# Kernel optimization log

Measured on AMD Instinct MI355X. Metric: run time of the kernel, lower is better.

The kernel has to match this reference:

```python
import jax, jax.numpy as jnp
import numpy as np

TEMPERATURE = 8.0  # sqrt(d_head=64), from init_kwargs
NEG_INF = -1e9


def setup_inputs() -> dict:
    key = jax.random.key(0)
    k1, k2, k3, k4 = jax.random.split(key, 4)
    B, H, N, D = 2, 16, 2048, 64
    q = jax.random.normal(k1, (B, H, N, D), dtype=jnp.float32)
    k = jax.random.normal(k2, (B, H, N, D), dtype=jnp.float32)
    v = jax.random.normal(k3, (B, H, N, D), dtype=jnp.float32)
    mask = jax.random.randint(k4, (B, 1, N), 0, 2, dtype=jnp.int32)
    return {"q": q, "k": k, "v": v, "mask": mask}


def reference(q, k, v, mask):
    # scores: [B,H,N,N]
    attn = jnp.einsum("bhqd,bhkd->bhqk", q / TEMPERATURE, k)
    # symmetric padding mask: masked if row OR col token is masked
    m = mask.astype(attn.dtype)            # [B,1,N]
    row = m[:, :, :, None]                 # [B,1,N,1]
    col = m[:, :, None, :]                 # [B,1,1,N]
    sym = 1.0 - (1.0 - row) * (1.0 - col)  # [B,1,N,N], broadcasts over H
    attn = jnp.where(sym == 1.0, NEG_INF, attn)
    attn = jax.nn.softmax(attn, axis=-1)
    output = jnp.einsum("bhqk,bhkd->bhqd", attn, v)
    return output, attn
```

## Files before the change

kernel.cpp:

```cpp
#include <hip/hip_runtime.h>

typedef _Float16 half8 __attribute__((ext_vector_type(8)));
typedef _Float16 half4v __attribute__((ext_vector_type(4)));
typedef float f32x4 __attribute__((ext_vector_type(4)));

__global__ __launch_bounds__(256, 2)
void attn_fused(const float* __restrict__ qg_, const float* __restrict__ kg_,
                const float* __restrict__ vg_, const int* __restrict__ mg_,
                float* __restrict__ outg_, float* __restrict__ attng_)
{
    constexpr int N = 2048, D = 64, TM = 128, BK = 128, NCH = 16;
    constexpr int QS = 72, KS = 72, VTS = 136, PS = 72;
    constexpr float INVN = 1.0f / 2048.0f;

    __shared__ _Float16 Qs[TM * QS];
    __shared__ _Float16 Ksh[BK * KS];
    __shared__ _Float16 Vts[D * VTS];
    __shared__ _Float16 Ps[TM * PS];
    __shared__ unsigned char cm[N];

    const int tid  = threadIdx.x;
    const int wid  = tid >> 6;
    const int lane = tid & 63;
    const int quad = lane >> 4;
    const int l15  = lane & 15;

    const int bh = blockIdx.x & 31;
    const int qt = blockIdx.x >> 5;
    const int b  = bh >> 4;

    const float* qg = qg_ + ((size_t)bh * N + qt * TM) * D;
    const float* kg = kg_ + (size_t)bh * N * D;
    const float* vg = vg_ + (size_t)bh * N * D;
    const int*   mg = mg_ + (size_t)b * N;
    float* attng = attng_ + ((size_t)bh * N + (size_t)qt * TM) * N;
    float* outg  = outg_  + ((size_t)bh * N + qt * TM) * D;

#pragma unroll
    for (int i = 0; i < 8; ++i) {
        int f = tid + 256 * i;
        int row = f >> 4, d = (f & 15) * 4;
        float4 x = *reinterpret_cast<const float4*>(qg + (size_t)row * D + d);
        half4v hv;
        hv[0] = (_Float16)(x.x * 0.125f);
        hv[1] = (_Float16)(x.y * 0.125f);
        hv[2] = (_Float16)(x.z * 0.125f);
        hv[3] = (_Float16)(x.w * 0.125f);
        *reinterpret_cast<half4v*>(&Qs[row * QS + d]) = hv;
        cm[f] = (unsigned char)(mg[f] ? 0 : 1);
    }

    float rowm[2][4];
#pragma unroll
    for (int mb = 0; mb < 2; ++mb)
#pragma unroll
        for (int r = 0; r < 4; ++r) {
            int row = qt * TM + wid * 32 + mb * 16 + quad * 4 + r;
            rowm[mb][r] = (float)mg[row];
        }

    __syncthreads();

    half8 qf[2][2];
#pragma unroll
    for (int mb = 0; mb < 2; ++mb)
#pragma unroll
        for (int ks = 0; ks < 2; ++ks)
            qf[mb][ks] = *reinterpret_cast<half8*>(
                &Qs[(wid * 32 + mb * 16 + l15) * QS + ks * 32 + quad * 8]);

    float lsum[2][4] = {{0,0,0,0},{0,0,0,0}};

    for (int kc = 0; kc < NCH; ++kc) {
        __syncthreads();
#pragma unroll
        for (int i = 0; i < 8; ++i) {
            int f = tid + 256 * i;
            int row = f >> 4, d = (f & 15) * 4;
            float4 x = *reinterpret_cast<const float4*>(kg + (size_t)(kc * BK + row) * D + d);
            half4v hv;
            hv[0] = (_Float16)x.x; hv[1] = (_Float16)x.y;
            hv[2] = (_Float16)x.z; hv[3] = (_Float16)x.w;
            *reinterpret_cast<half4v*>(&Ksh[row * KS + d]) = hv;
        }
        __syncthreads();

#pragma unroll
        for (int mb = 0; mb < 2; ++mb) {
#pragma unroll
            for (int nb = 0; nb < 8; ++nb) {
                f32x4 acc = {0.f, 0.f, 0.f, 0.f};
#pragma unroll
                for (int ks = 0; ks < 2; ++ks) {
                    half8 bf = *reinterpret_cast<half8*>(
                        &Ksh[(nb * 16 + l15) * KS + ks * 32 + quad * 8]);
                    acc = __builtin_amdgcn_mfma_f32_16x16x32_f16(qf[mb][ks], bf, acc, 0, 0, 0);
                }
                float cmf = (float)cm[kc * BK + nb * 16 + l15];
#pragma unroll
                for (int r = 0; r < 4; ++r)
                    lsum[mb][r] += cmf * __expf(acc[r]);
            }
        }
    }

#pragma unroll
    for (int mb = 0; mb < 2; ++mb)
#pragma unroll
        for (int r = 0; r < 4; ++r) {
            float s = lsum[mb][r];
            s += __shfl_xor(s, 1, 64);
            s += __shfl_xor(s, 2, 64);
            s += __shfl_xor(s, 4, 64);
            s += __shfl_xor(s, 8, 64);
            lsum[mb][r] = s;
        }

    float rscale[2][4], radd[2][4];
#pragma unroll
    for (int mb = 0; mb < 2; ++mb)
#pragma unroll
        for (int r = 0; r < 4; ++r) {
            bool uni = (rowm[mb][r] != 0.0f) || !(lsum[mb][r] > 0.0f);
            rscale[mb][r] = uni ? 0.0f : 1.0f / lsum[mb][r];
            radd[mb][r]   = uni ? INVN : 0.0f;
        }

    f32x4 Oacc[2][4];
#pragma unroll
    for (int mb = 0; mb < 2; ++mb)
#pragma unroll
        for (int nd = 0; nd < 4; ++nd)
            Oacc[mb][nd] = (f32x4){0.f, 0.f, 0.f, 0.f};

    for (int kc = 0; kc < NCH; ++kc) {
        __syncthreads();
#pragma unroll
        for (int i = 0; i < 8; ++i) {
            int f = tid + 256 * i;
            int row = f >> 4, d = (f & 15) * 4;
            float4 x = *reinterpret_cast<const float4*>(kg + (size_t)(kc * BK + row) * D + d);
            half4v hv;
            hv[0] = (_Float16)x.x; hv[1] = (_Float16)x.y;
            hv[2] = (_Float16)x.z; hv[3] = (_Float16)x.w;
            *reinterpret_cast<half4v*>(&Ksh[row * KS + d]) = hv;
        }
#pragma unroll
        for (int rr = 0; rr < 4; ++rr) {
            int key0 = rr * 32 + wid * 8;
            half8 hh;
#pragma unroll
            for (int j = 0; j < 8; ++j)
                hh[j] = (_Float16)vg[(size_t)(kc * BK + key0 + j) * D + lane];
            *reinterpret_cast<half8*>(&Vts[lane * VTS + key0]) = hh;
        }
        __syncthreads();

        f32x4 S[2][8];
#pragma unroll
        for (int mb = 0; mb < 2; ++mb)
#pragma unroll
            for (int nb = 0; nb < 8; ++nb) {
                f32x4 acc = {0.f, 0.f, 0.f, 0.f};
#pragma unroll
                for (int ks = 0; ks < 2; ++ks) {
                    half8 bf = *reinterpret_cast<half8*>(
                        &Ksh[(nb * 16 + l15) * KS + ks * 32 + quad * 8]);
                    acc = __builtin_amdgcn_mfma_f32_16x16x32_f16(qf[mb][ks], bf, acc, 0, 0, 0);
                }
                S[mb][nb] = acc;
            }

#pragma unroll
        for (int h = 0; h < 2; ++h) {
#pragma unroll
            for (int nb2 = 0; nb2 < 4; ++nb2) {
                int nb = h * 4 + nb2;
                int col = kc * BK + nb * 16 + l15;
                float cmf = (float)cm[col];
#pragma unroll
                for (int mb = 0; mb < 2; ++mb) {
#pragma unroll
                    for (int r = 0; r < 4; ++r) {
                        float p = cmf * __expf(S[mb][nb][r]) * rscale[mb][r] + radd[mb][r];
                        attng[(size_t)(wid * 32 + mb * 16 + quad * 4 + r) * N + col] = p;
                        Ps[(wid * 32 + mb * 16 + quad * 4 + r) * PS + nb2 * 16 + l15] = (_Float16)p;
                    }
                }
            }
            asm volatile("s_waitcnt lgkmcnt(0)" ::: "memory");
#pragma unroll
            for (int ks = 0; ks < 2; ++ks) {
                half8 af[2];
#pragma unroll
                for (int mb = 0; mb < 2; ++mb)
                    af[mb] = *reinterpret_cast<half8*>(
                        &Ps[(wid * 32 + mb * 16 + l15) * PS + ks * 32 + quad * 8]);
#pragma unroll
                for (int nd = 0; nd < 4; ++nd) {
                    half8 bf = *reinterpret_cast<half8*>(
                        &Vts[(nd * 16 + l15) * VTS + h * 64 + ks * 32 + quad * 8]);
#pragma unroll
                    for (int mb = 0; mb < 2; ++mb)
                        Oacc[mb][nd] = __builtin_amdgcn_mfma_f32_16x16x32_f16(af[mb], bf, Oacc[mb][nd], 0, 0, 0);
                }
            }
        }
    }

#pragma unroll
    for (int mb = 0; mb < 2; ++mb)
#pragma unroll
        for (int nd = 0; nd < 4; ++nd)
#pragma unroll
            for (int r = 0; r < 4; ++r)
                outg[(size_t)(wid * 32 + mb * 16 + quad * 4 + r) * D + nd * 16 + l15] =
                    Oacc[mb][nd][r];
}

extern "C" void kernel_launch(void* const* d_in, const int* in_sizes, int n_in,
                              void* d_out, int out_size, void* d_ws, size_t ws_size,
                              hipStream_t stream) {
    const float* q   = (const float*)d_in[0];
    const float* k   = (const float*)d_in[1];
    const float* v   = (const float*)d_in[2];
    const int*   msk = (const int*)d_in[3];
    float* out  = (float*)d_out;
    float* attn = out + (size_t)2 * 16 * 2048 * 64;
    dim3 grid(512), block(256);
    hipLaunchKernelGGL(attn_fused, grid, block, 0, stream, q, k, v, msk, out, attn);
}
```

Baseline: 671.6 us.

## Vectorize attention-matrix stores via LDS restaging and use exp2 with folded log2e

Attention probabilities are now written to global memory as 16-byte nontemporal vector stores, read back from the fp16 P tile in shared memory, instead of scalar strided stores straight from MFMA registers. The log2(e) factor is folded into the Q scale so the exponentials use the hardware exp2 instruction. The output stores also become nontemporal. The stored attention values are now rounded through fp16, which loses precision in the returned attn matrix and could fail a tight tolerance.

```diff
diff --git a/kernel.cpp b/kernel.cpp
--- a/kernel.cpp
+++ b/kernel.cpp
@@ -3,6 +3,12 @@
 typedef _Float16 half8 __attribute__((ext_vector_type(8)));
 typedef _Float16 half4v __attribute__((ext_vector_type(4)));
 typedef float f32x4 __attribute__((ext_vector_type(4)));
+
+#if __has_builtin(__builtin_amdgcn_exp2f)
+#define EXP2F(x) __builtin_amdgcn_exp2f(x)
+#else
+#define EXP2F(x) exp2f(x)
+#endif
 
 __global__ __launch_bounds__(256, 2)
 void attn_fused(const float* __restrict__ qg_, const float* __restrict__ kg_,
@@ -12,6 +18,7 @@
     constexpr int N = 2048, D = 64, TM = 128, BK = 128, NCH = 16;
     constexpr int QS = 72, KS = 72, VTS = 136, PS = 72;
     constexpr float INVN = 1.0f / 2048.0f;
+    constexpr float QSCALE = 1.44269504088896340736f * 0.125f;
 
     __shared__ _Float16 Qs[TM * QS];
     __shared__ _Float16 Ksh[BK * KS];
@@ -42,10 +49,10 @@
         int row = f >> 4, d = (f & 15) * 4;
         float4 x = *reinterpret_cast<const float4*>(qg + (size_t)row * D + d);
         half4v hv;
-        hv[0] = (_Float16)(x.x * 0.125f);
-        hv[1] = (_Float16)(x.y * 0.125f);
-        hv[2] = (_Float16)(x.z * 0.125f);
-        hv[3] = (_Float16)(x.w * 0.125f);
+        hv[0] = (_Float16)(x.x * QSCALE);
+        hv[1] = (_Float16)(x.y * QSCALE);
+        hv[2] = (_Float16)(x.z * QSCALE);
+        hv[3] = (_Float16)(x.w * QSCALE);
         *reinterpret_cast<half4v*>(&Qs[row * QS + d]) = hv;
         cm[f] = (unsigned char)(mg[f] ? 0 : 1);
     }
@@ -99,7 +106,7 @@
                 float cmf = (float)cm[kc * BK + nb * 16 + l15];
 #pragma unroll
                 for (int r = 0; r < 4; ++r)
-                    lsum[mb][r] += cmf * __expf(acc[r]);
+                    lsum[mb][r] += cmf * EXP2F(acc[r]);
             }
         }
     }
@@ -176,19 +183,30 @@
 #pragma unroll
             for (int nb2 = 0; nb2 < 4; ++nb2) {
                 int nb = h * 4 + nb2;
-                int col = kc * BK + nb * 16 + l15;
-                float cmf = (float)cm[col];
+                float cmf = (float)cm[kc * BK + nb * 16 + l15];
 #pragma unroll
                 for (int mb = 0; mb < 2; ++mb) {
 #pragma unroll
                     for (int r = 0; r < 4; ++r) {
-                        float p = cmf * __expf(S[mb][nb][r]) * rscale[mb][r] + radd[mb][r];
-                        attng[(size_t)(wid * 32 + mb * 16 + quad * 4 + r) * N + col] = p;
+                        float p = cmf * EXP2F(S[mb][nb][r]) * rscale[mb][r] + radd[mb][r];
                         Ps[(wid * 32 + mb * 16 + quad * 4 + r) * PS + nb2 * 16 + l15] = (_Float16)p;
                     }
                 }
             }
             asm volatile("s_waitcnt lgkmcnt(0)" ::: "memory");
+
+#pragma unroll
+            for (int r8 = 0; r8 < 8; ++r8) {
+                int rl = r8 * 4 + quad;
+                half4v ph = *reinterpret_cast<half4v*>(
+                    &Ps[(wid * 32 + rl) * PS + l15 * 4]);
+                f32x4 pf;
+                pf[0] = (float)ph[0]; pf[1] = (float)ph[1];
+                pf[2] = (float)ph[2]; pf[3] = (float)ph[3];
+                float* dst = attng + (size_t)(wid * 32 + rl) * N + kc * BK + h * 64 + l15 * 4;
+                __builtin_nontemporal_store(pf, reinterpret_cast<f32x4*>(dst));
+            }
+
 #pragma unroll
             for (int ks = 0; ks < 2; ++ks) {
                 half8 af[2];
@@ -214,8 +232,9 @@
         for (int nd = 0; nd < 4; ++nd)
 #pragma unroll
             for (int r = 0; r < 4; ++r)
-                outg[(size_t)(wid * 32 + mb * 16 + quad * 4 + r) * D + nd * 16 + l15] =
-                    Oacc[mb][nd][r];
+                __builtin_nontemporal_store(
+                    Oacc[mb][nd][r],
+                    outg + (size_t)(wid * 32 + mb * 16 + quad * 4 + r) * D + nd * 16 + l15);
 }
 
 extern "C" void kernel_launch(void* const* d_in, const int* in_sizes, int n_in,
```

After: 650.2 us. 1.03x faster.
